# Optimization experiments

Hardware: AMD Instinct MI355X
Metric: run time of the kernel (lower is better)

Reference implementation:

```python
import jax, jax.numpy as jnp
import numpy as np

D_MODEL = 1024
NUM_HEADS = 16
HEAD_DIM = D_MODEL // NUM_HEADS


def setup_inputs() -> dict:
    key = jax.random.key(0)
    ks = jax.random.split(key, 9)
    s = 1.0 / np.sqrt(D_MODEL)
    x = jax.random.normal(ks[0], (4, 2048, D_MODEL), dtype=jnp.float32)
    Wq = jax.random.uniform(ks[1], (D_MODEL, D_MODEL), jnp.float32, -s, s)
    bq = jax.random.uniform(ks[2], (D_MODEL,), jnp.float32, -s, s)
    Wk = jax.random.uniform(ks[3], (D_MODEL, D_MODEL), jnp.float32, -s, s)
    bk = jax.random.uniform(ks[4], (D_MODEL,), jnp.float32, -s, s)
    Wv = jax.random.uniform(ks[5], (D_MODEL, D_MODEL), jnp.float32, -s, s)
    bv = jax.random.uniform(ks[6], (D_MODEL,), jnp.float32, -s, s)
    Wo = jax.random.uniform(ks[7], (D_MODEL, D_MODEL), jnp.float32, -s, s)
    bo = jax.random.uniform(ks[8], (D_MODEL,), jnp.float32, -s, s)
    return {"x": x, "Wq": Wq, "bq": bq, "Wk": Wk, "bk": bk,
            "Wv": Wv, "bv": bv, "Wo": Wo, "bo": bo}


def reference(x, Wq, bq, Wk, bk, Wv, bv, Wo, bo):
    B, S, D = x.shape
    H, hd = NUM_HEADS, HEAD_DIM
    # QKV projections (torch Linear: x @ W^T + b)
    q = (x @ Wq.T + bq).reshape(B, S, H, hd).transpose(0, 2, 1, 3)  # [B,H,S,hd]
    k = (x @ Wk.T + bk).reshape(B, S, H, hd).transpose(0, 2, 1, 3)
    v = (x @ Wv.T + bv).reshape(B, S, H, hd).transpose(0, 2, 1, 3)
    scores = jnp.einsum('bhqd,bhkd->bhqk', q, k) / jnp.sqrt(jnp.float32(hd))
    attn = jax.nn.softmax(scores, axis=-1)  # dropout is identity in eval
    ctx = jnp.einsum('bhqk,bhkd->bhqd', attn, v)
    ctx = ctx.transpose(0, 2, 1, 3).reshape(B, S, D)
    return ctx @ Wo.T + bo
```

## Files before the change

kernel.cpp:

```cpp
#include <hip/hip_runtime.h>

typedef __bf16 bf16;
typedef __bf16 bf16x4 __attribute__((ext_vector_type(4)));
typedef __bf16 bf16x8 __attribute__((ext_vector_type(8)));
typedef float  f32x4  __attribute__((ext_vector_type(4)));
typedef float  f32x16 __attribute__((ext_vector_type(16)));
typedef unsigned int u32x4v __attribute__((ext_vector_type(4)));

#define NB   4
#define SEQ  2048
#define DM   1024
#define NH   16
#define HD   64
#define BHN  (NB*NH)
#define MTOT (NB*SEQ)
#define ELEMS ((size_t)MTOT*DM)
#define WELEMS (DM*DM)
#define QSCALE 0.18033688011112042f

__device__ __forceinline__ void gload16(void* lds, const void* g) {
  __builtin_amdgcn_global_load_lds(
      (const __attribute__((address_space(1))) void*)g,
      (__attribute__((address_space(3))) void*)lds, 16, 0, 0);
}

__device__ __forceinline__ f32x4 mfma16(bf16x8 a, bf16x8 b, f32x4 c) {
  return __builtin_amdgcn_mfma_f32_16x16x32_bf16(a, b, c, 0, 0, 0);
}
__device__ __forceinline__ f32x16 mfma32(bf16x8 a, bf16x8 b, f32x16 c) {
  return __builtin_amdgcn_mfma_f32_32x32x16_bf16(a, b, c, 0, 0, 0);
}
__device__ __forceinline__ unsigned cvtpk(float lo, float hi) {
  unsigned r;
  asm("v_cvt_pk_bf16_f32 %0, %1, %2" : "=v"(r) : "v"(lo), "v"(hi));
  return r;
}
__device__ __forceinline__ float exp2a(float x) {
  float r;
  asm("v_exp_f32 %0, %1" : "=v"(r) : "v"(x));
  return r;
}

__global__ __launch_bounds__(256) void cvt_all(
    const float* __restrict__ x, bf16* __restrict__ xb,
    const float* __restrict__ w0, const float* __restrict__ w1,
    const float* __restrict__ w2, const float* __restrict__ w3,
    bf16* __restrict__ wb)
{
  int y = blockIdx.y;
  const float* src; bf16* dst; int nblk;
  if (y < 4) {
    src = (y == 0) ? w0 : (y == 1) ? w1 : (y == 2) ? w2 : w3;
    dst = wb + (size_t)y * WELEMS;
    nblk = WELEMS / 1024;
  } else {
    src = x; dst = xb; nblk = (int)(ELEMS / 1024);
  }
  if (blockIdx.x >= nblk) return;
  int i = blockIdx.x * 1024 + threadIdx.x * 4;
  f32x4 v = *(const f32x4*)(src + i);
  bf16x4 o;
#pragma unroll
  for (int j = 0; j < 4; j++) o[j] = (bf16)v[j];
  *(bf16x4*)(dst + i) = o;
}


__global__ __launch_bounds__(512, 2) void gemm_qkv256(
    const bf16* __restrict__ A, const bf16* __restrict__ Wb3,
    const float* __restrict__ bq, const float* __restrict__ bk,
    const float* __restrict__ bv,
    bf16* __restrict__ Qb, bf16* __restrict__ Kb, bf16* __restrict__ Vtb)
{
  __shared__ __align__(16) bf16 la[2][256*64];
  __shared__ __align__(16) bf16 lb[2][128*64];

  const int K = 1024;
  int tid = threadIdx.x, wid = tid >> 6, lane = tid & 63;
  int wr = wid >> 1, wc = wid & 1;
  int c15 = lane & 15, hi = lane >> 4, l7 = lane & 7;

  int orig = blockIdx.x;
  int xcd = orig & 7, j = orig >> 3;
  int by = xcd * 4 + (j & 3);
  int bx = j >> 2;
  int m0 = by * 256, n0 = bx * 128;
  int z  = n0 >> 10;
  const float* bias = (z == 0) ? bq : (z == 1) ? bk : bv;

  int r8 = lane >> 3;
  int cu = (lane & 7) ^ r8;

  const bf16* gA = A   + (size_t)m0 * K;
  const bf16* gW = Wb3 + (size_t)n0 * K;

#define STA(buf, h, kt)                                                        \
  {                                                                            \
    _Pragma("unroll")                                                          \
    for (int op = 0; op < 2; op++) {                                           \
      int rowl = (h)*128 + wid*16 + op*8 + r8;                                 \
      gload16(&la[buf][((h)*128 + wid*16 + op*8)*64],                          \
              gA + (size_t)rowl*K + (kt)*64 + cu*8);                           \
    }                                                                          \
  }
#define STB(buf, kt)                                                           \
  {                                                                            \
    _Pragma("unroll")                                                          \
    for (int op = 0; op < 2; op++) {                                           \
      int rowl = wid*16 + op*8 + r8;                                           \
      gload16(&lb[buf][(wid*16 + op*8)*64],                                    \
              gW + (size_t)rowl*K + (kt)*64 + cu*8);                           \
    }                                                                          \
  }

  f32x4 acc[4][4] = {};
  const int NT = K / 64;

  STB(0, 0);
  STA(0, 0, 0);
  STA(0, 1, 0);

  for (int t = 0; t < NT; ++t) {
    int cb = t & 1, nb = cb ^ 1;
    asm volatile("s_waitcnt vmcnt(2)" ::: "memory");
    __builtin_amdgcn_s_barrier();
    asm volatile("" ::: "memory");

    bf16x8 af0[2][2], af1[2][2], bf0[2][2], bf1[2][2];

#pragma unroll
    for (int mi = 0; mi < 2; mi++)
#pragma unroll
      for (int kk = 0; kk < 2; kk++)
        af0[mi][kk] = *(const bf16x8*)(&la[cb][(wr*32 + mi*16 + c15)*64 + (((kk*4 + hi) ^ l7) * 8)]);
#pragma unroll
    for (int ni = 0; ni < 2; ni++)
#pragma unroll
      for (int kk = 0; kk < 2; kk++)
        bf0[ni][kk] = *(const bf16x8*)(&lb[cb][(wc*64 + ni*16 + c15)*64 + (((kk*4 + hi) ^ l7) * 8)]);
    if (t + 1 < NT) STB(nb, t + 1);
    __builtin_amdgcn_s_setprio(1);
#pragma unroll
    for (int mi = 0; mi < 2; mi++)
#pragma unroll
      for (int ni = 0; ni < 2; ni++)
#pragma unroll
        for (int kk = 0; kk < 2; kk++)
          acc[mi][ni] = mfma16(af0[mi][kk], bf0[ni][kk], acc[mi][ni]);
    __builtin_amdgcn_s_setprio(0);

#pragma unroll
    for (int ni = 0; ni < 2; ni++)
#pragma unroll
      for (int kk = 0; kk < 2; kk++)
        bf1[ni][kk] = *(const bf16x8*)(&lb[cb][(wc*64 + 32 + ni*16 + c15)*64 + (((kk*4 + hi) ^ l7) * 8)]);
    if (t + 1 < NT) STA(nb, 0, t + 1);
    __builtin_amdgcn_s_setprio(1);
#pragma unroll
    for (int mi = 0; mi < 2; mi++)
#pragma unroll
      for (int ni = 0; ni < 2; ni++)
#pragma unroll
        for (int kk = 0; kk < 2; kk++)
          acc[mi][2 + ni] = mfma16(af0[mi][kk], bf1[ni][kk], acc[mi][2 + ni]);
    __builtin_amdgcn_s_setprio(0);

    if (t + 1 < NT) { asm volatile("s_waitcnt vmcnt(4)" ::: "memory"); }
    else            { asm volatile("s_waitcnt vmcnt(0)" ::: "memory"); }
    __builtin_amdgcn_s_barrier();
    asm volatile("" ::: "memory");

#pragma unroll
    for (int mi = 0; mi < 2; mi++)
#pragma unroll
      for (int kk = 0; kk < 2; kk++)
        af1[mi][kk] = *(const bf16x8*)(&la[cb][(128 + wr*32 + mi*16 + c15)*64 + (((kk*4 + hi) ^ l7) * 8)]);
    if (t + 1 < NT) STA(nb, 1, t + 1);
    __builtin_amdgcn_s_setprio(1);
#pragma unroll
    for (int mi = 0; mi < 2; mi++)
#pragma unroll
      for (int ni = 0; ni < 2; ni++)
#pragma unroll
        for (int kk = 0; kk < 2; kk++)
          acc[2 + mi][2 + ni] = mfma16(af1[mi][kk], bf1[ni][kk], acc[2 + mi][2 + ni]);
    __builtin_amdgcn_s_setprio(0);

    __builtin_amdgcn_s_setprio(1);
#pragma unroll
    for (int mi = 0; mi < 2; mi++)
#pragma unroll
      for (int ni = 0; ni < 2; ni++)
#pragma unroll
        for (int kk = 0; kk < 2; kk++)
          acc[2 + mi][ni] = mfma16(af1[mi][kk], bf0[ni][kk], acc[2 + mi][ni]);
    __builtin_amdgcn_s_setprio(0);
  }
#undef STA
#undef STB

#pragma unroll
  for (int mi = 0; mi < 4; mi++) {
    int rbase = m0 + ((mi < 2) ? (wr*32 + mi*16) : (128 + wr*32 + (mi - 2)*16)) + hi*4;
#pragma unroll
    for (int ni = 0; ni < 4; ni++) {
      int n  = n0 + wc*64 + ni*16 + c15;
      int cz = n & 1023;
      float bvv = bias[cz];
      int h = cz >> 6, d = cz & 63;
      int b = rbase >> 11, s = rbase & 2047;
      if (z < 2) {
        bf16* C = z ? Kb : Qb;
        float sc = z ? 1.0f : QSCALE;
#pragma unroll
        for (int r = 0; r < 4; r++)
          C[((b*NH + h)*SEQ + (s + r))*HD + d] = (bf16)((acc[mi][ni][r] + bvv) * sc);
      } else {
        bf16x4 o;
#pragma unroll
        for (int r = 0; r < 4; r++) o[r] = (bf16)(acc[mi][ni][r] + bvv);
        *(bf16x4*)(Vtb + ((size_t)(b*NH + h)*HD + d)*SEQ + s) = o;
      }
    }
  }
}

__global__ __launch_bounds__(512, 2) void gemm_out256(
    const bf16* __restrict__ A, const bf16* __restrict__ W,
    const float* __restrict__ bias, float* __restrict__ C)
{
  __shared__ __align__(16) bf16 la[2][256*64];
  __shared__ __align__(16) bf16 lb[2][128*64];

  const int K = 1024;
  int tid = threadIdx.x, wid = tid >> 6, lane = tid & 63;
  int wr = wid >> 1, wc = wid & 1;
  int c15 = lane & 15, hi = lane >> 4, l7 = lane & 7;

  int orig = blockIdx.x;
  int xcd = orig & 7, j = orig >> 3;
  int by = xcd * 4 + (j & 3);
  int bx = j >> 2;
  int m0 = by * 256, n0 = bx * 128;

  int r8 = lane >> 3;
  int cu = (lane & 7) ^ r8;

  const bf16* gA = A + (size_t)m0 * K;
  const bf16* gW = W + (size_t)n0 * K;

#define STA(buf, h, kt)                                                        \
  {                                                                            \
    _Pragma("unroll")                                                          \
    for (int op = 0; op < 2; op++) {                                           \
      int rowl = (h)*128 + wid*16 + op*8 + r8;                                 \
      gload16(&la[buf][((h)*128 + wid*16 + op*8)*64],                          \
              gA + (size_t)rowl*K + (kt)*64 + cu*8);                           \
    }                                                                          \
  }
#define STB(buf, kt)                                                           \
  {                                                                            \
    _Pragma("unroll")                                                          \
    for (int op = 0; op < 2; op++) {                                           \
      int rowl = wid*16 + op*8 + r8;                                           \
      gload16(&lb[buf][(wid*16 + op*8)*64],                                    \
              gW + (size_t)rowl*K + (kt)*64 + cu*8);                           \
    }                                                                          \
  }

  f32x4 acc[4][4] = {};
  const int NT = K / 64;

  STB(0, 0);
  STA(0, 0, 0);
  STA(0, 1, 0);

  for (int t = 0; t < NT; ++t) {
    int cb = t & 1, nb = cb ^ 1;
    asm volatile("s_waitcnt vmcnt(2)" ::: "memory");
    __builtin_amdgcn_s_barrier();
    asm volatile("" ::: "memory");

    bf16x8 af0[2][2], af1[2][2], bf0[2][2], bf1[2][2];

#pragma unroll
    for (int mi = 0; mi < 2; mi++)
#pragma unroll
      for (int kk = 0; kk < 2; kk++)
        af0[mi][kk] = *(const bf16x8*)(&la[cb][(wr*32 + mi*16 + c15)*64 + (((kk*4 + hi) ^ l7) * 8)]);
#pragma unroll
    for (int ni = 0; ni < 2; ni++)
#pragma unroll
      for (int kk = 0; kk < 2; kk++)
        bf0[ni][kk] = *(const bf16x8*)(&lb[cb][(wc*64 + ni*16 + c15)*64 + (((kk*4 + hi) ^ l7) * 8)]);
    if (t + 1 < NT) STB(nb, t + 1);
    __builtin_amdgcn_s_setprio(1);
#pragma unroll
    for (int mi = 0; mi < 2; mi++)
#pragma unroll
      for (int ni = 0; ni < 2; ni++)
#pragma unroll
        for (int kk = 0; kk < 2; kk++)
          acc[mi][ni] = mfma16(af0[mi][kk], bf0[ni][kk], acc[mi][ni]);
    __builtin_amdgcn_s_setprio(0);

#pragma unroll
    for (int ni = 0; ni < 2; ni++)
#pragma unroll
      for (int kk = 0; kk < 2; kk++)
        bf1[ni][kk] = *(const bf16x8*)(&lb[cb][(wc*64 + 32 + ni*16 + c15)*64 + (((kk*4 + hi) ^ l7) * 8)]);
    if (t + 1 < NT) STA(nb, 0, t + 1);
    __builtin_amdgcn_s_setprio(1);
#pragma unroll
    for (int mi = 0; mi < 2; mi++)
#pragma unroll
      for (int ni = 0; ni < 2; ni++)
#pragma unroll
        for (int kk = 0; kk < 2; kk++)
          acc[mi][2 + ni] = mfma16(af0[mi][kk], bf1[ni][kk], acc[mi][2 + ni]);
    __builtin_amdgcn_s_setprio(0);

    if (t + 1 < NT) { asm volatile("s_waitcnt vmcnt(4)" ::: "memory"); }
    else            { asm volatile("s_waitcnt vmcnt(0)" ::: "memory"); }
    __builtin_amdgcn_s_barrier();
    asm volatile("" ::: "memory");

#pragma unroll
    for (int mi = 0; mi < 2; mi++)
#pragma unroll
      for (int kk = 0; kk < 2; kk++)
        af1[mi][kk] = *(const bf16x8*)(&la[cb][(128 + wr*32 + mi*16 + c15)*64 + (((kk*4 + hi) ^ l7) * 8)]);
    if (t + 1 < NT) STA(nb, 1, t + 1);
    __builtin_amdgcn_s_setprio(1);
#pragma unroll
    for (int mi = 0; mi < 2; mi++)
#pragma unroll
      for (int ni = 0; ni < 2; ni++)
#pragma unroll
        for (int kk = 0; kk < 2; kk++)
          acc[2 + mi][2 + ni] = mfma16(af1[mi][kk], bf1[ni][kk], acc[2 + mi][2 + ni]);
    __builtin_amdgcn_s_setprio(0);

    __builtin_amdgcn_s_setprio(1);
#pragma unroll
    for (int mi = 0; mi < 2; mi++)
#pragma unroll
      for (int ni = 0; ni < 2; ni++)
#pragma unroll
        for (int kk = 0; kk < 2; kk++)
          acc[2 + mi][ni] = mfma16(af1[mi][kk], bf0[ni][kk], acc[2 + mi][ni]);
    __builtin_amdgcn_s_setprio(0);
  }
#undef STA
#undef STB

#pragma unroll
  for (int mi = 0; mi < 4; mi++) {
    int rbase = m0 + ((mi < 2) ? (wr*32 + mi*16) : (128 + wr*32 + (mi - 2)*16)) + hi*4;
#pragma unroll
    for (int ni = 0; ni < 4; ni++) {
      int col = n0 + wc*64 + ni*16 + c15;
      float bvv = bias[col];
#pragma unroll
      for (int r = 0; r < 4; r++)
        C[(size_t)(rbase + r)*DM + col] = acc[mi][ni][r] + bvv;
    }
  }
}

__global__ __launch_bounds__(256, 2) void attn(
    const bf16* __restrict__ Q, const bf16* __restrict__ Kin,
    const bf16* __restrict__ Vt, bf16* __restrict__ ctx)
{
  __shared__ __align__(16) bf16 kt[2][128*64];
  __shared__ __align__(16) bf16 vt[2][64*128];

  int tid = threadIdx.x, wid = tid >> 6, lane = tid & 63;
  int l31 = lane & 31, hi = lane >> 5, l7 = lane & 7;

  int orig = blockIdx.y * gridDim.x + blockIdx.x;
  int swz  = (orig & 7) * 64 + (orig >> 3);
  int bh   = swz >> 3, q0 = (swz & 7) * 256;

  const bf16* Qp = Q   + (size_t)bh*SEQ*HD;
  const bf16* Kp = Kin + (size_t)bh*SEQ*HD;
  const bf16* Vp = Vt  + (size_t)bh*HD*SEQ;
  int qw = q0 + wid*64;

  bf16x8 qf[2][4];
#pragma unroll
  for (int qt = 0; qt < 2; qt++)
#pragma unroll
    for (int dblk = 0; dblk < 4; dblk++)
      qf[qt][dblk] = *(const bf16x8*)(Qp + (size_t)(qw + qt*32 + l31)*HD + dblk*16 + hi*8);

  f32x16 po[2][2]  = {};
  f32x16 posum[2]  = {};

  bf16x8 onesv;
#pragma unroll
  for (int j = 0; j < 8; j++) onesv[j] = (bf16)1.0f;

  int r8 = lane >> 3;
  int ck = (lane & 7) ^ r8;
  int r16 = lane >> 4, c16v = lane & 15;

#define STAGE(buf, kv0)                                                        \
  {                                                                            \
    _Pragma("unroll")                                                          \
    for (int op = 0; op < 4; op++) {                                           \
      int rk = wid*32 + op*8 + r8;                                             \
      gload16(&kt[buf][(wid*32 + op*8)*64],                                    \
              Kp + (size_t)((kv0) + rk)*HD + ck*8);                            \
      int rv = wid*16 + op*4 + r16;                                            \
      gload16(&vt[buf][(wid*16 + op*4)*128],                                   \
              Vp + (size_t)rv*SEQ + (kv0) + ((c16v ^ (rv & 7))*8));            \
    }                                                                          \
  }

  STAGE(0, 0);
  __syncthreads();

  for (int it = 0; it < SEQ/128; ++it) {
    int cur = it & 1;
    if (it < SEQ/128 - 1) STAGE(cur ^ 1, (it + 1) * 128);

#pragma unroll
    for (int sub = 0; sub < 2; sub++) {
      f32x16 st[2][2] = {};
      __builtin_amdgcn_s_setprio(1);
#pragma unroll
      for (int kvt = 0; kvt < 2; kvt++) {
        int rowb = (sub*64 + kvt*32 + l31) * 64;
#pragma unroll
        for (int dblk = 0; dblk < 4; dblk++) {
          bf16x8 kf = *(const bf16x8*)(&kt[cur][rowb + (((dblk*2 + hi) ^ l7) * 8)]);
          st[0][kvt] = mfma32(kf, qf[0][dblk], st[0][kvt]);
          st[1][kvt] = mfma32(kf, qf[1][dblk], st[1][kvt]);
        }
      }
      __builtin_amdgcn_s_setprio(0);

      bf16x8 pa[2][2][2];
#pragma unroll
      for (int qt = 0; qt < 2; qt++) {
#pragma unroll
        for (int kvt = 0; kvt < 2; kvt++)
#pragma unroll
          for (int i = 0; i < 16; i++)
            st[qt][kvt][i] = exp2a(st[qt][kvt][i]);
#pragma unroll
        for (int kvt = 0; kvt < 2; kvt++)
#pragma unroll
          for (int cp = 0; cp < 2; cp++) {
            int m0 = 2*cp, m1 = 2*cp + 1;
            unsigned w0a = cvtpk(st[qt][kvt][4*m0+0], st[qt][kvt][4*m0+1]);
            unsigned w1a = cvtpk(st[qt][kvt][4*m0+2], st[qt][kvt][4*m0+3]);
            unsigned w0b = cvtpk(st[qt][kvt][4*m1+0], st[qt][kvt][4*m1+1]);
            unsigned w1b = cvtpk(st[qt][kvt][4*m1+2], st[qt][kvt][4*m1+3]);
            asm("v_permlane32_swap_b32 %0, %1" : "+v"(w0a), "+v"(w0b));
            asm("v_permlane32_swap_b32 %0, %1" : "+v"(w1a), "+v"(w1b));
            pa[qt][kvt][cp] = __builtin_bit_cast(bf16x8, (u32x4v){w0a, w1a, w0b, w1b});
          }
      }

      __builtin_amdgcn_s_setprio(1);
#pragma unroll
      for (int dt = 0; dt < 2; dt++) {
        int rowb = (dt*32 + l31) * 128;
#pragma unroll
        for (int c = 0; c < 4; c++) {
          bf16x8 vf = *(const bf16x8*)(&vt[cur][rowb + ((sub*8 + ((c*2 + hi) ^ l7)) * 8)]);
          po[0][dt] = mfma32(pa[0][c >> 1][c & 1], vf, po[0][dt]);
          po[1][dt] = mfma32(pa[1][c >> 1][c & 1], vf, po[1][dt]);
        }
      }
#pragma unroll
      for (int c = 0; c < 4; c++) {
        posum[0] = mfma32(pa[0][c >> 1][c & 1], onesv, posum[0]);
        posum[1] = mfma32(pa[1][c >> 1][c & 1], onesv, posum[1]);
      }
      __builtin_amdgcn_s_setprio(0);
    }

    __syncthreads();
  }
#undef STAGE

  int b = bh >> 4, h = bh & 15;
#pragma unroll
  for (int qt = 0; qt < 2; qt++)
#pragma unroll
    for (int reg = 0; reg < 16; reg++) {
      int qq = (reg & 3) + 8*(reg >> 2) + 4*hi;
      float inv = 1.0f / posum[qt][reg];
      int s = qw + qt*32 + qq;
      bf16* dst = ctx + (size_t)(b*SEQ + s)*DM + h*HD + l31;
      dst[0]  = (bf16)(po[qt][0][reg] * inv);
      dst[32] = (bf16)(po[qt][1][reg] * inv);
    }
}

extern "C" void kernel_launch(void* const* d_in, const int* in_sizes, int n_in,
                              void* d_out, int out_size, void* d_ws, size_t ws_size,
                              hipStream_t stream)
{
  const float* x  = (const float*)d_in[0];
  const float* Wq = (const float*)d_in[1];
  const float* bq = (const float*)d_in[2];
  const float* Wk = (const float*)d_in[3];
  const float* bk = (const float*)d_in[4];
  const float* Wv = (const float*)d_in[5];
  const float* bv = (const float*)d_in[6];
  const float* Wo = (const float*)d_in[7];
  const float* bo = (const float*)d_in[8];

  bf16* ws  = (bf16*)d_ws;
  bf16* xb  = ws;
  bf16* Wb  = ws + ELEMS;
  bf16* Qb  = ws + ELEMS + 4*WELEMS;
  bf16* Kb  = Qb + ELEMS;
  bf16* Vtb = Kb + ELEMS;
  bf16* ctx = xb;

  cvt_all<<<dim3(ELEMS/1024, 5), dim3(256), 0, stream>>>(x, xb, Wq, Wk, Wv, Wo, Wb);
  gemm_qkv256<<<dim3(768), dim3(512), 0, stream>>>(
      xb, Wb, bq, bk, bv, Qb, Kb, Vtb);
  attn<<<dim3(SEQ/256, BHN), dim3(256), 0, stream>>>(Qb, Kb, Vtb, ctx);
  gemm_out256<<<dim3(256), dim3(512), 0, stream>>>(
      ctx, Wb + 3*WELEMS, bo, (float*)d_out);
}
```

Measured before the change: 179.0 us.

## Fuse fp32-to-bf16 conversion of x into QKV GEMM A-tile loads

Removes the separate pass that converts x to bf16. The QKV GEMM now reads fp32 x directly into registers, packs it to bf16 and writes swizzled tiles into LDS, prefetching two k-tiles ahead. This drops a full write and re-read of the bf16 copy of x. In exchange it doubles the global bytes the GEMM reads for A, uses more registers, and replaces async global-to-LDS loads with register staging under a reworked wait/barrier schedule, leaving one barrier per k-iteration.

```diff
diff --git a/kernel.cpp b/kernel.cpp
--- a/kernel.cpp
+++ b/kernel.cpp
@@ -5,6 +5,7 @@
 typedef __bf16 bf16x8 __attribute__((ext_vector_type(8)));
 typedef float  f32x4  __attribute__((ext_vector_type(4)));
 typedef float  f32x16 __attribute__((ext_vector_type(16)));
+typedef unsigned int u32x2 __attribute__((ext_vector_type(2)));
 typedef unsigned int u32x4v __attribute__((ext_vector_type(4)));
 
 #define NB   4
@@ -41,22 +42,14 @@
   return r;
 }
 
-__global__ __launch_bounds__(256) void cvt_all(
-    const float* __restrict__ x, bf16* __restrict__ xb,
+__global__ __launch_bounds__(256) void cvt_w(
     const float* __restrict__ w0, const float* __restrict__ w1,
     const float* __restrict__ w2, const float* __restrict__ w3,
     bf16* __restrict__ wb)
 {
   int y = blockIdx.y;
-  const float* src; bf16* dst; int nblk;
-  if (y < 4) {
-    src = (y == 0) ? w0 : (y == 1) ? w1 : (y == 2) ? w2 : w3;
-    dst = wb + (size_t)y * WELEMS;
-    nblk = WELEMS / 1024;
-  } else {
-    src = x; dst = xb; nblk = (int)(ELEMS / 1024);
-  }
-  if (blockIdx.x >= nblk) return;
+  const float* src = (y == 0) ? w0 : (y == 1) ? w1 : (y == 2) ? w2 : w3;
+  bf16* dst = wb + (size_t)y * WELEMS;
   int i = blockIdx.x * 1024 + threadIdx.x * 4;
   f32x4 v = *(const f32x4*)(src + i);
   bf16x4 o;
@@ -65,9 +58,8 @@
   *(bf16x4*)(dst + i) = o;
 }
 
-
 __global__ __launch_bounds__(512, 2) void gemm_qkv256(
-    const bf16* __restrict__ A, const bf16* __restrict__ Wb3,
+    const float* __restrict__ Ax, const bf16* __restrict__ Wb3,
     const float* __restrict__ bq, const float* __restrict__ bk,
     const float* __restrict__ bv,
     bf16* __restrict__ Qb, bf16* __restrict__ Kb, bf16* __restrict__ Vtb)
@@ -91,16 +83,29 @@
   int r8 = lane >> 3;
   int cu = (lane & 7) ^ r8;
 
-  const bf16* gA = A   + (size_t)m0 * K;
-  const bf16* gW = Wb3 + (size_t)n0 * K;
-
-#define STA(buf, h, kt)                                                        \
+  const float* gA = Ax  + (size_t)m0 * K;
+  const bf16*  gW = Wb3 + (size_t)n0 * K;
+
+  int arow_lo = lane >> 4;
+  int acol4   = (lane & 15) * 4;
+  int k2      = (lane & 15) >> 1;
+  int ksub    = lane & 1;
+
+#define LDA(kt)                                                                \
   {                                                                            \
     _Pragma("unroll")                                                          \
-    for (int op = 0; op < 2; op++) {                                           \
-      int rowl = (h)*128 + wid*16 + op*8 + r8;                                 \
-      gload16(&la[buf][((h)*128 + wid*16 + op*8)*64],                          \
-              gA + (size_t)rowl*K + (kt)*64 + cu*8);                           \
+    for (int i = 0; i < 8; i++)                                                \
+      areg[i] = *(const f32x4*)(gA + (size_t)(wid*32 + i*4 + arow_lo)*K        \
+                                  + (kt)*64 + acol4);                          \
+  }
+#define CVTWR(buf)                                                             \
+  {                                                                            \
+    _Pragma("unroll")                                                          \
+    for (int i = 0; i < 8; i++) {                                              \
+      int row = wid*32 + i*4 + arow_lo;                                        \
+      u32x2 w = { cvtpk(areg[i][0], areg[i][1]),                               \
+                  cvtpk(areg[i][2], areg[i][3]) };                             \
+      *(u32x2*)(&la[buf][row*64 + ((k2 ^ (row & 7)) * 8) + ksub*4]) = w;       \
     }                                                                          \
   }
 #define STB(buf, kt)                                                           \
@@ -113,18 +118,21 @@
     }                                                                          \
   }
 
+  f32x4 areg[8];
   f32x4 acc[4][4] = {};
   const int NT = K / 64;
 
+  LDA(0);
+  CVTWR(0);
   STB(0, 0);
-  STA(0, 0, 0);
-  STA(0, 1, 0);
+  LDA(1);
+  asm volatile("s_waitcnt vmcnt(8)" ::: "memory");
+  asm volatile("s_waitcnt lgkmcnt(0)" ::: "memory");
+  __builtin_amdgcn_s_barrier();
+  asm volatile("" ::: "memory");
 
   for (int t = 0; t < NT; ++t) {
     int cb = t & 1, nb = cb ^ 1;
-    asm volatile("s_waitcnt vmcnt(2)" ::: "memory");
-    __builtin_amdgcn_s_barrier();
-    asm volatile("" ::: "memory");
 
     bf16x8 af0[2][2], af1[2][2], bf0[2][2], bf1[2][2];
 
@@ -154,7 +162,6 @@
 #pragma unroll
       for (int kk = 0; kk < 2; kk++)
         bf1[ni][kk] = *(const bf16x8*)(&lb[cb][(wc*64 + 32 + ni*16 + c15)*64 + (((kk*4 + hi) ^ l7) * 8)]);
-    if (t + 1 < NT) STA(nb, 0, t + 1);
     __builtin_amdgcn_s_setprio(1);
 #pragma unroll
     for (int mi = 0; mi < 2; mi++)
@@ -165,17 +172,11 @@
           acc[mi][2 + ni] = mfma16(af0[mi][kk], bf1[ni][kk], acc[mi][2 + ni]);
     __builtin_amdgcn_s_setprio(0);
 
-    if (t + 1 < NT) { asm volatile("s_waitcnt vmcnt(4)" ::: "memory"); }
-    else            { asm volatile("s_waitcnt vmcnt(0)" ::: "memory"); }
-    __builtin_amdgcn_s_barrier();
-    asm volatile("" ::: "memory");
-
 #pragma unroll
     for (int mi = 0; mi < 2; mi++)
 #pragma unroll
       for (int kk = 0; kk < 2; kk++)
         af1[mi][kk] = *(const bf16x8*)(&la[cb][(128 + wr*32 + mi*16 + c15)*64 + (((kk*4 + hi) ^ l7) * 8)]);
-    if (t + 1 < NT) STA(nb, 1, t + 1);
     __builtin_amdgcn_s_setprio(1);
 #pragma unroll
     for (int mi = 0; mi < 2; mi++)
@@ -195,8 +196,22 @@
         for (int kk = 0; kk < 2; kk++)
           acc[2 + mi][ni] = mfma16(af1[mi][kk], bf0[ni][kk], acc[2 + mi][ni]);
     __builtin_amdgcn_s_setprio(0);
-  }
-#undef STA
+
+    if (t + 1 < NT) {
+      CVTWR(nb);
+      if (t + 2 < NT) {
+        LDA(t + 2);
+        asm volatile("s_waitcnt vmcnt(8)" ::: "memory");
+      } else {
+        asm volatile("s_waitcnt vmcnt(0)" ::: "memory");
+      }
+      asm volatile("s_waitcnt lgkmcnt(0)" ::: "memory");
+      __builtin_amdgcn_s_barrier();
+      asm volatile("" ::: "memory");
+    }
+  }
+#undef LDA
+#undef CVTWR
 #undef STB
 
 #pragma unroll
@@ -516,16 +531,15 @@
   const float* bo = (const float*)d_in[8];
 
   bf16* ws  = (bf16*)d_ws;
-  bf16* xb  = ws;
+  bf16* ctx = ws;
   bf16* Wb  = ws + ELEMS;
   bf16* Qb  = ws + ELEMS + 4*WELEMS;
   bf16* Kb  = Qb + ELEMS;
   bf16* Vtb = Kb + ELEMS;
-  bf16* ctx = xb;
-
-  cvt_all<<<dim3(ELEMS/1024, 5), dim3(256), 0, stream>>>(x, xb, Wq, Wk, Wv, Wo, Wb);
+
+  cvt_w<<<dim3(WELEMS/1024, 4), dim3(256), 0, stream>>>(Wq, Wk, Wv, Wo, Wb);
   gemm_qkv256<<<dim3(768), dim3(512), 0, stream>>>(
-      xb, Wb, bq, bk, bv, Qb, Kb, Vtb);
+      x, Wb, bq, bk, bv, Qb, Kb, Vtb);
   attn<<<dim3(SEQ/256, BHN), dim3(256), 0, stream>>>(Qb, Kb, Vtb, ctx);
   gemm_out256<<<dim3(256), dim3(512), 0, stream>>>(
       ctx, Wb + 3*WELEMS, bo, (float*)d_out);
```

After: 174.8 us, median of 2. 2.4% less time.
